# Performance work log

Measured on AMD Instinct MI355X. Metric: run time of the kernel, lower is better.

## Reference

```python
import jax, jax.numpy as jnp
import numpy as np

GROUPS = 3
EPS = 1e-5


def grouped_conv1x1(x, w, groups):
    # x: [B, Cin, H, W], w: [Cout, Cin//groups] (1x1 kernel flattened)
    B, Cin, H, W = x.shape
    Cout = w.shape[0]
    xg = x.reshape(B, groups, Cin // groups, H, W)
    wg = w.reshape(groups, Cout // groups, Cin // groups)
    yg = jnp.einsum('bgihw,goi->bgohw', xg, wg)
    return yg.reshape(B, Cout, H, W)


def depthwise_conv3x3(x, w):
    # x: [B, C, H, W], w: [C, 1, 3, 3]; stride 1, padding 1
    C = x.shape[1]
    return jax.lax.conv_general_dilated(
        x, w, window_strides=(1, 1), padding=((1, 1), (1, 1)),
        dimension_numbers=('NCHW', 'OIHW', 'NCHW'), feature_group_count=C)


def batchnorm(x, gamma, beta, mean, var):
    inv = gamma * jax.lax.rsqrt(var + EPS)
    return x * inv[None, :, None, None] + (beta - mean * inv)[None, :, None, None]


def channel_shuffle(x, groups):
    B, C, H, W = x.shape
    return x.reshape(B, groups, C // groups, H, W).transpose(0, 2, 1, 3, 4).reshape(B, C, H, W)


def setup_inputs() -> dict:
    key = jax.random.key(0)
    ks = jax.random.split(key, 12)
    B, Cin, H, W = 32, 240, 56, 56
    Cout = 240
    mid = Cout // 4  # 60
    inp = {
        'x': jax.random.normal(ks[0], (B, Cin, H, W), jnp.float32),
        'w1': jax.random.normal(ks[1], (mid, Cin // GROUPS), jnp.float32) * 0.05,
        'g1': jax.random.normal(ks[2], (mid,), jnp.float32) * 0.1 + 1.0,
        'b1': jax.random.normal(ks[3], (mid,), jnp.float32) * 0.1,
        'm1': jax.random.normal(ks[4], (mid,), jnp.float32) * 0.1,
        'v1': jax.random.uniform(ks[5], (mid,), jnp.float32, 0.5, 1.5),
        'w2': jax.random.normal(ks[6], (mid, 1, 3, 3), jnp.float32) * 0.1,
        'g2': jnp.ones((mid,), jnp.float32),
        'b2': jnp.zeros((mid,), jnp.float32),
        'm2': jax.random.normal(ks[7], (mid,), jnp.float32) * 0.1,
        'v2': jax.random.uniform(ks[8], (mid,), jnp.float32, 0.5, 1.5),
        'w3': jax.random.normal(ks[9], (Cout, mid // GROUPS), jnp.float32) * 0.05,
        'g3': jax.random.normal(ks[10], (Cout,), jnp.float32) * 0.1 + 1.0,
        'b3': jnp.zeros((Cout,), jnp.float32),
        'm3': jax.random.normal(ks[11], (Cout,), jnp.float32) * 0.1,
        'v3': jnp.ones((Cout,), jnp.float32),
    }
    return inp


def reference(x, w1, g1, b1, m1, v1, w2, g2, b2, m2, v2, w3, g3, b3, m3, v3):
    out = grouped_conv1x1(x, w1, GROUPS)
    out = jax.nn.relu(batchnorm(out, g1, b1, m1, v1))
    out = depthwise_conv3x3(out, w2)
    out = batchnorm(out, g2, b2, m2, v2)
    out = channel_shuffle(out, GROUPS)
    out = grouped_conv1x1(out, w3, GROUPS)
    out = jax.nn.relu(batchnorm(out, g3, b3, m3, v3))
    # in_channels == out_channels -> identity shortcut
    return out + x
```

## Files before the change

kernel.cpp:

```cpp
#include <hip/hip_runtime.h>

#define BN_EPS 1e-5f
#define WW 56
#define HWSZ 3136
#define NB 32
#define CIN 240
#define MID 60
#define MIDG 20
#define COUT 240
#define COUTG 80
#define TH 7
#define THH 9

__global__ __launch_bounds__(512, 2) void kA_conv1_dw(
        const float* __restrict__ x,
        const float* __restrict__ w1, const float* __restrict__ g1,
        const float* __restrict__ b1, const float* __restrict__ m1,
        const float* __restrict__ v1,
        const float* __restrict__ w2, const float* __restrict__ g2,
        const float* __restrict__ b2, const float* __restrict__ m2,
        const float* __restrict__ v2,
        float* __restrict__ t2) {
    __shared__ float mid[MIDG * THH * WW];
    __shared__ float w1s[MIDG * 80];
    __shared__ float w2s[MIDG * 9];
    __shared__ float shA[MIDG], shB[MIDG];

    const int tid = threadIdx.x;
    const int bid = blockIdx.x;
    const int t   = bid & 7;
    const int gb  = bid >> 3;
    const int g   = gb % 3;
    const int b   = gb / 3;
    const int h0  = t * TH;

    for (int i = tid; i < MIDG * 80; i += 512) {
        int chg = g * MIDG + i / 80;
        w1s[i] = w1[chg * 80 + i % 80] * (g1[chg] * rsqrtf(v1[chg] + BN_EPS));
    }
    for (int i = tid; i < MIDG * 9; i += 512) {
        int chg = g * MIDG + i / 9;
        w2s[i] = w2[chg * 9 + i % 9] * (g2[chg] * rsqrtf(v2[chg] + BN_EPS));
    }
    if (tid < MIDG) {
        int chg = g * MIDG + tid;
        float s1v = g1[chg] * rsqrtf(v1[chg] + BN_EPS);
        shA[tid] = b1[chg] - m1[chg] * s1v;
        float s2v = g2[chg] * rsqrtf(v2[chg] + BN_EPS);
        shB[tid] = b2[chg] - m2[chg] * s2v;
    }
    __syncthreads();

    {
        const int q   = tid & 3;
        const int idx = tid >> 2;
        if (idx < 126) {
            const int r  = idx / 14, c4 = idx % 14;
            const int hh = h0 - 1 + r;
            float4 acc[5];
#pragma unroll
            for (int c = 0; c < 5; c++) acc[c] = make_float4(0.f, 0.f, 0.f, 0.f);
            if (hh >= 0 && hh < 56) {
                const float* xp = x + ((size_t)(b * CIN + g * 80)) * HWSZ + hh * WW + c4 * 4;
                const float4* w4 = (const float4*)w1s;
#pragma unroll 4
                for (int ci4 = 0; ci4 < 20; ci4++) {
                    float4 xv0 = *(const float4*)(xp + (ci4 * 4 + 0) * HWSZ);
                    float4 xv1 = *(const float4*)(xp + (ci4 * 4 + 1) * HWSZ);
                    float4 xv2 = *(const float4*)(xp + (ci4 * 4 + 2) * HWSZ);
                    float4 xv3 = *(const float4*)(xp + (ci4 * 4 + 3) * HWSZ);
#pragma unroll
                    for (int c = 0; c < 5; c++) {
                        float4 wv = w4[(q * 5 + c) * 20 + ci4];
                        acc[c].x += wv.x * xv0.x + wv.y * xv1.x + wv.z * xv2.x + wv.w * xv3.x;
                        acc[c].y += wv.x * xv0.y + wv.y * xv1.y + wv.z * xv2.y + wv.w * xv3.y;
                        acc[c].z += wv.x * xv0.z + wv.y * xv1.z + wv.z * xv2.z + wv.w * xv3.z;
                        acc[c].w += wv.x * xv0.w + wv.y * xv1.w + wv.z * xv2.w + wv.w * xv3.w;
                    }
                }
#pragma unroll
                for (int c = 0; c < 5; c++) {
                    float s = shA[q * 5 + c];
                    acc[c].x = fmaxf(acc[c].x + s, 0.f);
                    acc[c].y = fmaxf(acc[c].y + s, 0.f);
                    acc[c].z = fmaxf(acc[c].z + s, 0.f);
                    acc[c].w = fmaxf(acc[c].w + s, 0.f);
                }
            }
#pragma unroll
            for (int c = 0; c < 5; c++)
                *(float4*)(mid + ((q * 5 + c) * THH + r) * WW + c4 * 4) = acc[c];
        }
    }
    __syncthreads();

#pragma unroll
    for (int k = 0; k < 4; k++) {
        const int it = tid + k * 512;
        if (it < MIDG * 98) {
            const int ch = it / 98;
            const int pq = it % 98;
            const int r = pq / 14, c4 = pq % 14;
            const float* base = mid + ch * (THH * WW);
            const float* kw = w2s + ch * 9;
            float4 a = make_float4(0.f, 0.f, 0.f, 0.f);
#pragma unroll
            for (int dy = 0; dy < 3; dy++) {
                const float* row = base + (r + dy) * WW + c4 * 4;
                float4 m = *(const float4*)row;
                float l  = (c4 > 0)  ? row[-1] : 0.f;
                float rt = (c4 < 13) ? row[4]  : 0.f;
                const float k0 = kw[dy * 3 + 0];
                const float k1 = kw[dy * 3 + 1];
                const float k2 = kw[dy * 3 + 2];
                a.x += k0 * l   + k1 * m.x + k2 * m.y;
                a.y += k0 * m.x + k1 * m.y + k2 * m.z;
                a.z += k0 * m.y + k1 * m.z + k2 * m.w;
                a.w += k0 * m.z + k1 * m.w + k2 * rt;
            }
            const float s = shB[ch];
            a.x += s; a.y += s; a.z += s; a.w += s;
            const int jj = ch * 3 + g;
            *(float4*)(t2 + ((size_t)(b * MID + jj)) * HWSZ + (h0 + r) * WW + c4 * 4) = a;
        }
    }
}

__global__ __launch_bounds__(256) void kB_conv3_res(
        const float* __restrict__ t2, const float* __restrict__ w3,
        const float* __restrict__ g3, const float* __restrict__ b3,
        const float* __restrict__ m3, const float* __restrict__ v3,
        const float* __restrict__ x, float* __restrict__ out) {
    __shared__ float wT[3 * MIDG * COUTG];
    __shared__ float s3[COUT], sh3[COUT];
    const int tid = threadIdx.x;
    for (int i = tid; i < 3 * MIDG * COUTG; i += 256) {
        int co_glob = i / MIDG;
        int ci = i % MIDG;
        int gg = co_glob / COUTG;
        int cg = co_glob % COUTG;
        wT[(gg * MIDG + ci) * COUTG + cg] = w3[i];
    }
    if (tid < COUT) {
        float inv = g3[tid] * rsqrtf(v3[tid] + BN_EPS);
        s3[tid] = inv;
        sh3[tid] = b3[tid] - m3[tid] * inv;
    }
    __syncthreads();

    const int item = blockIdx.x * 256 + tid;
    const unsigned q  = (unsigned)item & 3u;
    const unsigned pg = (unsigned)item >> 2;
    const unsigned p4 = pg % 784u;
    const unsigned bg = pg / 784u;
    const unsigned b = bg / 3u, g = bg % 3u;
    const int pos = (int)p4 * 4;

    float4 acc[MIDG];
#pragma unroll
    for (int c = 0; c < MIDG; c++) acc[c] = make_float4(0.f, 0.f, 0.f, 0.f);

    const float4* wl4 = (const float4*)wT;
#pragma unroll 4
    for (int ci = 0; ci < MIDG; ci++) {
        int csh = (int)g * MIDG + ci;
        float4 xv = *(const float4*)(t2 + ((size_t)(b * MID + csh)) * HWSZ + pos);
        int wbase = (csh * COUTG + q * MIDG) / 4;
#pragma unroll
        for (int k4 = 0; k4 < 5; k4++) {
            float4 wv = wl4[wbase + k4];
            acc[k4 * 4 + 0].x += wv.x * xv.x; acc[k4 * 4 + 0].y += wv.x * xv.y;
            acc[k4 * 4 + 0].z += wv.x * xv.z; acc[k4 * 4 + 0].w += wv.x * xv.w;
            acc[k4 * 4 + 1].x += wv.y * xv.x; acc[k4 * 4 + 1].y += wv.y * xv.y;
            acc[k4 * 4 + 1].z += wv.y * xv.z; acc[k4 * 4 + 1].w += wv.y * xv.w;
            acc[k4 * 4 + 2].x += wv.z * xv.x; acc[k4 * 4 + 2].y += wv.z * xv.y;
            acc[k4 * 4 + 2].z += wv.z * xv.z; acc[k4 * 4 + 2].w += wv.z * xv.w;
            acc[k4 * 4 + 3].x += wv.w * xv.x; acc[k4 * 4 + 3].y += wv.w * xv.y;
            acc[k4 * 4 + 3].z += wv.w * xv.z; acc[k4 * 4 + 3].w += wv.w * xv.w;
        }
    }

#pragma unroll
    for (int co = 0; co < MIDG; co++) {
        int cg = (int)g * COUTG + (int)q * MIDG + co;
        float sc = s3[cg], sf = sh3[cg];
        float4 xr = *(const float4*)(x + ((size_t)(b * CIN + cg)) * HWSZ + pos);
        float4 o;
        o.x = fmaxf(acc[co].x * sc + sf, 0.f) + xr.x;
        o.y = fmaxf(acc[co].y * sc + sf, 0.f) + xr.y;
        o.z = fmaxf(acc[co].z * sc + sf, 0.f) + xr.z;
        o.w = fmaxf(acc[co].w * sc + sf, 0.f) + xr.w;
        *(float4*)(out + ((size_t)(b * COUT + cg)) * HWSZ + pos) = o;
    }
}

extern "C" void kernel_launch(void* const* d_in, const int* in_sizes, int n_in,
                              void* d_out, int out_size, void* d_ws, size_t ws_size,
                              hipStream_t stream) {
    const float* x  = (const float*)d_in[0];
    const float* w1 = (const float*)d_in[1];
    const float* g1 = (const float*)d_in[2];
    const float* b1 = (const float*)d_in[3];
    const float* m1 = (const float*)d_in[4];
    const float* v1 = (const float*)d_in[5];
    const float* w2 = (const float*)d_in[6];
    const float* g2 = (const float*)d_in[7];
    const float* b2 = (const float*)d_in[8];
    const float* m2 = (const float*)d_in[9];
    const float* v2 = (const float*)d_in[10];
    const float* w3 = (const float*)d_in[11];
    const float* g3 = (const float*)d_in[12];
    const float* b3 = (const float*)d_in[13];
    const float* m3 = (const float*)d_in[14];
    const float* v3 = (const float*)d_in[15];
    float* out = (float*)d_out;

    float* t2 = (float*)d_ws;

    kA_conv1_dw<<<768, 512, 0, stream>>>(x, w1, g1, b1, m1, v1,
                                         w2, g2, b2, m2, v2, t2);
    kB_conv3_res<<<1176, 256, 0, stream>>>(t2, w3, g3, b3, m3, v3, x, out);
}
```

Before: 84.16 us.

## Stage input tile in shared memory in channel chunks for conv1

The first grouped 1x1 conv now loads the x tile into shared memory in four chunks of 20 input channels using all threads cooperatively. Previously each group of 4 threads read the same x values straight from global memory. Conv1 weights are now read from global memory, where they are likely cached, instead of a pre-scaled shared copy, and the BN1 scale is applied after accumulation. This uses more shared memory (an extra ~40KB tile) and adds syncs per chunk, which may reduce occupancy below the 2 blocks per CU that launch_bounds requests.

```diff
diff --git a/kernel.cpp b/kernel.cpp
--- a/kernel.cpp
+++ b/kernel.cpp
@@ -21,10 +21,10 @@
         const float* __restrict__ b2, const float* __restrict__ m2,
         const float* __restrict__ v2,
         float* __restrict__ t2) {
+    __shared__ float xt[MIDG * THH * WW];
     __shared__ float mid[MIDG * THH * WW];
-    __shared__ float w1s[MIDG * 80];
     __shared__ float w2s[MIDG * 9];
-    __shared__ float shA[MIDG], shB[MIDG];
+    __shared__ float shB[MIDG];
 
     const int tid = threadIdx.x;
     const int bid = blockIdx.x;
@@ -34,62 +34,80 @@
     const int b   = gb / 3;
     const int h0  = t * TH;
 
-    for (int i = tid; i < MIDG * 80; i += 512) {
-        int chg = g * MIDG + i / 80;
-        w1s[i] = w1[chg * 80 + i % 80] * (g1[chg] * rsqrtf(v1[chg] + BN_EPS));
-    }
-    for (int i = tid; i < MIDG * 9; i += 512) {
-        int chg = g * MIDG + i / 9;
-        w2s[i] = w2[chg * 9 + i % 9] * (g2[chg] * rsqrtf(v2[chg] + BN_EPS));
+    if (tid < MIDG * 9) {
+        int chg = g * MIDG + tid / 9;
+        w2s[tid] = w2[chg * 9 + tid % 9] * (g2[chg] * rsqrtf(v2[chg] + BN_EPS));
     }
     if (tid < MIDG) {
         int chg = g * MIDG + tid;
-        float s1v = g1[chg] * rsqrtf(v1[chg] + BN_EPS);
-        shA[tid] = b1[chg] - m1[chg] * s1v;
-        float s2v = g2[chg] * rsqrtf(v2[chg] + BN_EPS);
-        shB[tid] = b2[chg] - m2[chg] * s2v;
-    }
-    __syncthreads();
-
-    {
-        const int q   = tid & 3;
-        const int idx = tid >> 2;
-        if (idx < 126) {
-            const int r  = idx / 14, c4 = idx % 14;
-            const int hh = h0 - 1 + r;
-            float4 acc[5];
-#pragma unroll
-            for (int c = 0; c < 5; c++) acc[c] = make_float4(0.f, 0.f, 0.f, 0.f);
-            if (hh >= 0 && hh < 56) {
-                const float* xp = x + ((size_t)(b * CIN + g * 80)) * HWSZ + hh * WW + c4 * 4;
-                const float4* w4 = (const float4*)w1s;
-#pragma unroll 4
-                for (int ci4 = 0; ci4 < 20; ci4++) {
-                    float4 xv0 = *(const float4*)(xp + (ci4 * 4 + 0) * HWSZ);
-                    float4 xv1 = *(const float4*)(xp + (ci4 * 4 + 1) * HWSZ);
-                    float4 xv2 = *(const float4*)(xp + (ci4 * 4 + 2) * HWSZ);
-                    float4 xv3 = *(const float4*)(xp + (ci4 * 4 + 3) * HWSZ);
-#pragma unroll
-                    for (int c = 0; c < 5; c++) {
-                        float4 wv = w4[(q * 5 + c) * 20 + ci4];
-                        acc[c].x += wv.x * xv0.x + wv.y * xv1.x + wv.z * xv2.x + wv.w * xv3.x;
-                        acc[c].y += wv.x * xv0.y + wv.y * xv1.y + wv.z * xv2.y + wv.w * xv3.y;
-                        acc[c].z += wv.x * xv0.z + wv.y * xv1.z + wv.z * xv2.z + wv.w * xv3.z;
-                        acc[c].w += wv.x * xv0.w + wv.y * xv1.w + wv.z * xv2.w + wv.w * xv3.w;
-                    }
+        float s2 = g2[chg] * rsqrtf(v2[chg] + BN_EPS);
+        shB[tid] = b2[chg] - m2[chg] * s2;
+    }
+
+    const int q   = tid & 3;
+    const int idx = tid >> 2;
+    const int r   = idx / 14, c4 = idx % 14;
+    const bool act  = idx < 126;
+    const int  hh   = h0 - 1 + r;
+    const bool vrow = (hh >= 0 && hh < 56);
+
+    float4 acc[5];
+#pragma unroll
+    for (int c = 0; c < 5; c++) acc[c] = make_float4(0.f, 0.f, 0.f, 0.f);
+
+    const float* xg = x + ((size_t)(b * CIN + g * 80)) * HWSZ;
+
+    for (int chunk = 0; chunk < 4; ++chunk) {
+        if (chunk) __syncthreads();
+#pragma unroll
+        for (int k = 0; k < 5; k++) {
+            int i = tid + k * 512;
+            if (i < 2520) {
+                int ci  = i / 126;
+                int rem = i % 126;
+                int rr = rem / 14, cc = rem % 14;
+                int h2 = h0 - 1 + rr;
+                float4 v = make_float4(0.f, 0.f, 0.f, 0.f);
+                if (h2 >= 0 && h2 < 56)
+                    v = *(const float4*)(xg + (size_t)(chunk * 20 + ci) * HWSZ + h2 * WW + cc * 4);
+                *(float4*)(xt + (ci * THH + rr) * WW + cc * 4) = v;
+            }
+        }
+        __syncthreads();
+        if (act) {
+            const float* wrow = w1 + (size_t)(g * MIDG + q * 5) * 80 + chunk * 20;
+#pragma unroll
+            for (int ci4 = 0; ci4 < 5; ci4++) {
+                float4 xv0 = *(const float4*)(xt + ((ci4 * 4 + 0) * THH + r) * WW + c4 * 4);
+                float4 xv1 = *(const float4*)(xt + ((ci4 * 4 + 1) * THH + r) * WW + c4 * 4);
+                float4 xv2 = *(const float4*)(xt + ((ci4 * 4 + 2) * THH + r) * WW + c4 * 4);
+                float4 xv3 = *(const float4*)(xt + ((ci4 * 4 + 3) * THH + r) * WW + c4 * 4);
+#pragma unroll
+                for (int c = 0; c < 5; c++) {
+                    float4 wv = *(const float4*)(wrow + c * 80 + ci4 * 4);
+                    acc[c].x += wv.x * xv0.x + wv.y * xv1.x + wv.z * xv2.x + wv.w * xv3.x;
+                    acc[c].y += wv.x * xv0.y + wv.y * xv1.y + wv.z * xv2.y + wv.w * xv3.y;
+                    acc[c].z += wv.x * xv0.z + wv.y * xv1.z + wv.z * xv2.z + wv.w * xv3.z;
+                    acc[c].w += wv.x * xv0.w + wv.y * xv1.w + wv.z * xv2.w + wv.w * xv3.w;
                 }
-#pragma unroll
-                for (int c = 0; c < 5; c++) {
-                    float s = shA[q * 5 + c];
-                    acc[c].x = fmaxf(acc[c].x + s, 0.f);
-                    acc[c].y = fmaxf(acc[c].y + s, 0.f);
-                    acc[c].z = fmaxf(acc[c].z + s, 0.f);
-                    acc[c].w = fmaxf(acc[c].w + s, 0.f);
-                }
-            }
-#pragma unroll
-            for (int c = 0; c < 5; c++)
-                *(float4*)(mid + ((q * 5 + c) * THH + r) * WW + c4 * 4) = acc[c];
+            }
+        }
+    }
+
+    if (act) {
+#pragma unroll
+        for (int c = 0; c < 5; c++) {
+            int chg = g * MIDG + q * 5 + c;
+            float s1v = g1[chg] * rsqrtf(v1[chg] + BN_EPS);
+            float sh1v = b1[chg] - m1[chg] * s1v;
+            float4 res = make_float4(0.f, 0.f, 0.f, 0.f);
+            if (vrow) {
+                res.x = fmaxf(acc[c].x * s1v + sh1v, 0.f);
+                res.y = fmaxf(acc[c].y * s1v + sh1v, 0.f);
+                res.z = fmaxf(acc[c].z * s1v + sh1v, 0.f);
+                res.w = fmaxf(acc[c].w * s1v + sh1v, 0.f);
+            }
+            *(float4*)(mid + ((q * 5 + c) * THH + r) * WW + c4 * 4) = res;
         }
     }
     __syncthreads();
@@ -100,16 +118,16 @@
         if (it < MIDG * 98) {
             const int ch = it / 98;
             const int pq = it % 98;
-            const int r = pq / 14, c4 = pq % 14;
+            const int r2 = pq / 14, cc = pq % 14;
             const float* base = mid + ch * (THH * WW);
             const float* kw = w2s + ch * 9;
             float4 a = make_float4(0.f, 0.f, 0.f, 0.f);
 #pragma unroll
             for (int dy = 0; dy < 3; dy++) {
-                const float* row = base + (r + dy) * WW + c4 * 4;
+                const float* row = base + (r2 + dy) * WW + cc * 4;
                 float4 m = *(const float4*)row;
-                float l  = (c4 > 0)  ? row[-1] : 0.f;
-                float rt = (c4 < 13) ? row[4]  : 0.f;
+                float l  = (cc > 0)  ? row[-1] : 0.f;
+                float rt = (cc < 13) ? row[4]  : 0.f;
                 const float k0 = kw[dy * 3 + 0];
                 const float k1 = kw[dy * 3 + 1];
                 const float k2 = kw[dy * 3 + 2];
@@ -121,7 +139,7 @@
             const float s = shB[ch];
             a.x += s; a.y += s; a.z += s; a.w += s;
             const int jj = ch * 3 + g;
-            *(float4*)(t2 + ((size_t)(b * MID + jj)) * HWSZ + (h0 + r) * WW + c4 * 4) = a;
+            *(float4*)(t2 + ((size_t)(b * MID + jj)) * HWSZ + (h0 + r2) * WW + cc * 4) = a;
         }
     }
 }
@@ -190,7 +208,7 @@
         o.y = fmaxf(acc[co].y * sc + sf, 0.f) + xr.y;
         o.z = fmaxf(acc[co].z * sc + sf, 0.f) + xr.z;
         o.w = fmaxf(acc[co].w * sc + sf, 0.f) + xr.w;
-        *(float4*)(out + ((size_t)(b * COUT + cg)) * HWSZ + pos) = o;
+        *(float4*)(out + ((size_t)(b * CIN + cg)) * HWSZ + pos) = o;
     }
 }
 
```

Result: slower. 123.7 us (+47.0%).
